# Performance work log

Measured on AMD Instinct MI355X. Metric: run time of the kernel, lower is better.

The kernel has to match this reference:

```python
import jax, jax.numpy as jnp
import numpy as np

N = 6144          # nodes
F_IN = 512        # num_feature
HID = 64          # hidden_dim
C = 40            # num_class
H = 3             # num_heads
ALPHA = 0.2       # leaky relu slope
NEG_INF = -9e15


def gat_layer(x, adj, W, a_src, a_dst):
    # x: [N, f_in], W: [H, f_in, f_out], a_src/a_dst: [H, f_out]
    Wh = jnp.einsum('nf,hfo->hno', x, W)                  # [H, N, f_out]
    e_src = jnp.einsum('hno,ho->hn', Wh, a_src)           # [H, N]
    e_dst = jnp.einsum('hno,ho->hn', Wh, a_dst)           # [H, N]
    e = jax.nn.leaky_relu(e_src[:, :, None] + e_dst[:, None, :], ALPHA)  # [H, N, N]
    scores = jnp.where(adj > 0, e, NEG_INF)               # mask non-edges
    attn = jax.nn.softmax(scores, axis=-1)                # softmax over neighbors
    out = jnp.einsum('hnm,hmo->hno', attn, Wh)            # [H, N, f_out]
    return out.mean(axis=0)                               # average heads -> [N, f_out]


def setup_inputs() -> dict:
    key = jax.random.key(0)
    k = jax.random.split(key, 8)
    feature = jax.random.normal(k[0], (N, F_IN), dtype=jnp.float32)
    adj = (jax.random.uniform(k[1], (N, N)) < 0.01).astype(jnp.float32)
    adj = jnp.maximum(adj, jnp.eye(N, dtype=jnp.float32))
    s1 = 1.0 / np.sqrt(F_IN)
    s2 = 1.0 / np.sqrt(HID)
    W1 = jax.random.normal(k[2], (H, F_IN, HID), dtype=jnp.float32) * s1
    a1_src = jax.random.normal(k[3], (H, HID), dtype=jnp.float32) * s2
    a1_dst = jax.random.normal(k[4], (H, HID), dtype=jnp.float32) * s2
    W2 = jax.random.normal(k[5], (H, HID, C), dtype=jnp.float32) * s2
    a2_src = jax.random.normal(k[6], (H, C), dtype=jnp.float32) * (1.0 / np.sqrt(C))
    a2_dst = jax.random.normal(k[7], (H, C), dtype=jnp.float32) * (1.0 / np.sqrt(C))
    return {"feature": feature, "adj": adj, "W1": W1, "a1_src": a1_src,
            "a1_dst": a1_dst, "W2": W2, "a2_src": a2_src, "a2_dst": a2_dst}


def reference(feature, adj, W1, a1_src, a1_dst, W2, a2_src, a2_dst):
    # eval mode: dropout is identity
    x = jax.nn.relu(gat_layer(feature, adj, W1, a1_src, a1_dst))  # [N, HID]
    x = gat_layer(x, adj, W2, a2_src, a2_dst)                     # [N, C]
    return jax.nn.log_softmax(x, axis=1)
```

## Files before the change

kernel.cpp:

```cpp
#include <hip/hip_runtime.h>
#include <math.h>

#define NN   6144
#define FIN  512
#define HIDN 64
#define NC   40
#define NH   3
#define CAP  128
#define NCHUNK (CAP / 64)
#define LALPHA 0.2f
#define KSPLIT 4
#define PK_LOW  0x3FFFu
#define PK_HIGH 0xFFFFC000u

__global__ __launch_bounds__(256) void k_csr(const float* __restrict__ adj,
                                             int* __restrict__ nbr,
                                             int* __restrict__ deg) {
    int row  = blockIdx.x * 4 + (threadIdx.x >> 6);
    int lane = threadIdx.x & 63;
    const float* arow = adj + (size_t)row * NN;
    int* nrow = nbr + (size_t)row * CAP;
    int cnt = 0;
    for (int base = 0; base < NN; base += 256) {
        float4 v = *reinterpret_cast<const float4*>(arow + base + lane * 4);
        float vv[4] = {v.x, v.y, v.z, v.w};
#pragma unroll
        for (int q = 0; q < 4; q++) {
            bool on = vv[q] > 0.0f;
            unsigned long long mask = __ballot(on);
            if (on) {
                int pos = cnt + __popcll(mask & ((1ull << lane) - 1ull));
                if (pos < CAP) nrow[pos] = base + lane * 4 + q;
            }
            cnt += __popcll(mask);
        }
    }
    if (lane == 0) deg[row] = cnt < CAP ? cnt : CAP;
}

__global__ __launch_bounds__(256) void k_gemm1(const float* __restrict__ x,
                                               const float* __restrict__ W,
                                               float* __restrict__ Whp) {
    __shared__ float xs[64][68];
    __shared__ float wsh[64][68];
    int h  = blockIdx.y;
    int n0 = blockIdx.x * 64;
    int kz = blockIdx.z;
    int tid = threadIdx.x;
    int og4 = (tid & 15) * 4;
    int mg4 = (tid >> 4) * 4;

    float acc[4][4] = {{0.f}};

    const float* xbase0 = x + (size_t)n0 * FIN;
    const float* wbase0 = W + (size_t)h * FIN * HIDN;

    for (int t = 0; t < 2; t++) {
        int k0 = kz * 128 + t * 64;
#pragma unroll
        for (int i = 0; i < 4; i++) {
            int l = tid + i * 256;
            int r = l >> 4;
            int c = (l & 15) * 4;
            *reinterpret_cast<float4*>(&xs[r][c]) =
                *reinterpret_cast<const float4*>(xbase0 + (size_t)r * FIN + k0 + c);
            *reinterpret_cast<float4*>(&wsh[r][c]) =
                *reinterpret_cast<const float4*>(wbase0 + (size_t)(k0 + r) * HIDN + c);
        }
        __syncthreads();

#pragma unroll 8
        for (int k = 0; k < 64; k += 4) {
            float4 xv[4], wv[4];
            xv[0] = *reinterpret_cast<const float4*>(&xs[mg4 + 0][k]);
            xv[1] = *reinterpret_cast<const float4*>(&xs[mg4 + 1][k]);
            xv[2] = *reinterpret_cast<const float4*>(&xs[mg4 + 2][k]);
            xv[3] = *reinterpret_cast<const float4*>(&xs[mg4 + 3][k]);
            wv[0] = *reinterpret_cast<const float4*>(&wsh[k + 0][og4]);
            wv[1] = *reinterpret_cast<const float4*>(&wsh[k + 1][og4]);
            wv[2] = *reinterpret_cast<const float4*>(&wsh[k + 2][og4]);
            wv[3] = *reinterpret_cast<const float4*>(&wsh[k + 3][og4]);
            const float* xf = reinterpret_cast<const float*>(xv);
            const float* wf = reinterpret_cast<const float*>(wv);
#pragma unroll
            for (int i = 0; i < 4; i++) {
#pragma unroll
                for (int kk = 0; kk < 4; kk++) {
                    float xval = xf[i * 4 + kk];
#pragma unroll
                    for (int j = 0; j < 4; j++)
                        acc[i][j] += xval * wf[kk * 4 + j];
                }
            }
        }
        __syncthreads();
    }

    float* outp = Whp + (((size_t)kz * NH + h) * NN + n0 + mg4) * HIDN + og4;
#pragma unroll
    for (int i = 0; i < 4; i++) {
        float4 v = make_float4(acc[i][0], acc[i][1], acc[i][2], acc[i][3]);
        *reinterpret_cast<float4*>(outp + (size_t)i * HIDN) = v;
    }
}

__global__ __launch_bounds__(256) void k_sum_e1(const float* __restrict__ Whp,
                                                const float* __restrict__ a_src,
                                                const float* __restrict__ a_dst,
                                                float* __restrict__ Wh,
                                                float* __restrict__ es,
                                                float* __restrict__ ed) {
    int gw   = blockIdx.x * 4 + (threadIdx.x >> 6);
    int lane = threadIdx.x & 63;
    int h = gw / NN, n = gw % NN;
    size_t idx = ((size_t)h * NN + n) * HIDN + lane;
    size_t stride = (size_t)NH * NN * HIDN;
    float v = Whp[idx] + Whp[idx + stride] + Whp[idx + 2 * stride] + Whp[idx + 3 * stride];
    Wh[idx] = v;
    float s = v * a_src[h * HIDN + lane];
    float d = v * a_dst[h * HIDN + lane];
#pragma unroll
    for (int off = 32; off; off >>= 1) {
        s += __shfl_xor(s, off);
        d += __shfl_xor(d, off);
    }
    if (lane == 0) { es[h * NN + n] = s; ed[h * NN + n] = d; }
}

__global__ __launch_bounds__(192) void k_attn1f(const int* __restrict__ nbr,
                                                const int* __restrict__ deg,
                                                const float* __restrict__ Wh,
                                                const float* __restrict__ es,
                                                const float* __restrict__ ed,
                                                const float* __restrict__ W2,
                                                const float* __restrict__ a2s,
                                                const float* __restrict__ a2d,
                                                float* __restrict__ Wh2,
                                                float* __restrict__ e2s,
                                                float* __restrict__ e2d) {
    __shared__ unsigned pks[NH][CAP];
    __shared__ float hsum[NH][HIDN];
    int n = blockIdx.x;
    int h = threadIdx.x >> 6;
    int lane = threadIdx.x & 63;
    int d = deg[n];
    const int* nrow = nbr + (size_t)n * CAP;
    float esv = es[h * NN + n];

    float psum = 0.f;
#pragma unroll
    for (int c = 0; c < NCHUNK; c++) {
        int k = c * 64 + lane;
        unsigned u = 0;
        if (k < d) {
            int mm = nrow[k];
            float e = esv + ed[h * NN + mm];
            float s = e > 0.f ? e : LALPHA * e;
            float p = __expf(s);
            u = (__float_as_uint(p) & PK_HIGH) | (unsigned)mm;
            psum += __uint_as_float(u & PK_HIGH);
        }
        pks[h][k] = u;
    }
#pragma unroll
    for (int off = 32; off; off >>= 1) psum += __shfl_xor(psum, off);
    float inv = 1.f / psum;
    __syncthreads();

    const float* WhH = Wh + (size_t)h * NN * HIDN + lane;
    float a0 = 0.f, a1 = 0.f, a2 = 0.f, a3 = 0.f;
    int iters = (d + 3) >> 2;
    for (int g = 0; g < iters; g++) {
        uint4 uu = *reinterpret_cast<const uint4*>(&pks[h][g * 4]);
        a0 += __uint_as_float(uu.x & PK_HIGH) * WhH[(size_t)(uu.x & PK_LOW) * HIDN];
        a1 += __uint_as_float(uu.y & PK_HIGH) * WhH[(size_t)(uu.y & PK_LOW) * HIDN];
        a2 += __uint_as_float(uu.z & PK_HIGH) * WhH[(size_t)(uu.z & PK_LOW) * HIDN];
        a3 += __uint_as_float(uu.w & PK_HIGH) * WhH[(size_t)(uu.w & PK_LOW) * HIDN];
    }
    float hacc = ((a0 + a1) + (a2 + a3));
    hsum[h][lane] = hacc * inv;
    __syncthreads();

    float xv = (hsum[0][lane] + hsum[1][lane] + hsum[2][lane]) * (1.f / NH);
    xv = fmaxf(xv, 0.f);

    int c = lane < NC ? lane : NC - 1;
    float acc = 0.f;
#pragma unroll 8
    for (int o = 0; o < HIDN; o++) {
        float xb = __shfl(xv, o);
        float wv = W2[((size_t)h * HIDN + o) * NC + c];
        acc += xb * wv;
    }
    if (lane >= NC) acc = 0.f;

    float s2 = acc * (lane < NC ? a2s[h * NC + lane] : 0.f);
    float d2 = acc * (lane < NC ? a2d[h * NC + lane] : 0.f);
#pragma unroll
    for (int off = 32; off; off >>= 1) {
        s2 += __shfl_xor(s2, off);
        d2 += __shfl_xor(d2, off);
    }
    if (lane < NC) Wh2[((size_t)h * NN + n) * NC + lane] = acc;
    if (lane == 0) { e2s[h * NN + n] = s2; e2d[h * NN + n] = d2; }
}

__global__ __launch_bounds__(192) void k_attn2(const int* __restrict__ nbr,
                                               const int* __restrict__ deg,
                                               const float* __restrict__ Wh2,
                                               const float* __restrict__ es,
                                               const float* __restrict__ ed,
                                               float* __restrict__ out) {
    __shared__ unsigned pks[NH][CAP];
    __shared__ float hsum[NH][HIDN];
    int n = blockIdx.x;
    int h = threadIdx.x >> 6;
    int lane = threadIdx.x & 63;
    int d = deg[n];
    const int* nrow = nbr + (size_t)n * CAP;
    float esv = es[h * NN + n];

    float psum = 0.f;
#pragma unroll
    for (int c = 0; c < NCHUNK; c++) {
        int k = c * 64 + lane;
        unsigned u = 0;
        if (k < d) {
            int mm = nrow[k];
            float e = esv + ed[h * NN + mm];
            float s = e > 0.f ? e : LALPHA * e;
            float p = __expf(s);
            u = (__float_as_uint(p) & PK_HIGH) | (unsigned)mm;
            psum += __uint_as_float(u & PK_HIGH);
        }
        pks[h][k] = u;
    }
#pragma unroll
    for (int off = 32; off; off >>= 1) psum += __shfl_xor(psum, off);
    float inv = 1.f / psum;
    __syncthreads();

    const float* W2H = Wh2 + (size_t)h * NN * NC + (lane < NC ? lane : 0);
    float a0 = 0.f, a1 = 0.f, a2 = 0.f, a3 = 0.f;
    int iters = (d + 3) >> 2;
    for (int g = 0; g < iters; g++) {
        uint4 uu = *reinterpret_cast<const uint4*>(&pks[h][g * 4]);
        a0 += __uint_as_float(uu.x & PK_HIGH) * W2H[(size_t)(uu.x & PK_LOW) * NC];
        a1 += __uint_as_float(uu.y & PK_HIGH) * W2H[(size_t)(uu.y & PK_LOW) * NC];
        a2 += __uint_as_float(uu.z & PK_HIGH) * W2H[(size_t)(uu.z & PK_LOW) * NC];
        a3 += __uint_as_float(uu.w & PK_HIGH) * W2H[(size_t)(uu.w & PK_LOW) * NC];
    }
    float hacc = ((a0 + a1) + (a2 + a3));
    if (lane < NC) hsum[h][lane] = hacc * inv;
    __syncthreads();

    if (threadIdx.x < 64) {
        float a = (lane < NC)
            ? (hsum[0][lane] + hsum[1][lane] + hsum[2][lane]) * (1.f / NH)
            : -INFINITY;
        float mx = a;
#pragma unroll
        for (int off = 32; off; off >>= 1) mx = fmaxf(mx, __shfl_xor(mx, off));
        float ex = (lane < NC) ? __expf(a - mx) : 0.f;
        float se = ex;
#pragma unroll
        for (int off = 32; off; off >>= 1) se += __shfl_xor(se, off);
        if (lane < NC) out[(size_t)n * NC + lane] = a - mx - logf(se);
    }
}

extern "C" void kernel_launch(void* const* d_in, const int* in_sizes, int n_in,
                              void* d_out, int out_size, void* d_ws, size_t ws_size,
                              hipStream_t stream) {
    const float* feature = (const float*)d_in[0];
    const float* adj     = (const float*)d_in[1];
    const float* W1      = (const float*)d_in[2];
    const float* a1_src  = (const float*)d_in[3];
    const float* a1_dst  = (const float*)d_in[4];
    const float* W2      = (const float*)d_in[5];
    const float* a2_src  = (const float*)d_in[6];
    const float* a2_dst  = (const float*)d_in[7];
    float* out = (float*)d_out;

    char* ws = (char*)d_ws;
    size_t off = 0;
    int*   nbr = (int*)(ws + off);   off += (size_t)NN * CAP * sizeof(int);
    int*   deg = (int*)(ws + off);   off += (size_t)NN * sizeof(int);
    float* Whp = (float*)(ws + off); off += (size_t)KSPLIT * NH * NN * HIDN * sizeof(float);
    float* Wh1 = (float*)(ws + off); off += (size_t)NH * NN * HIDN * sizeof(float);
    float* e1s = (float*)(ws + off); off += (size_t)NH * NN * sizeof(float);
    float* e1d = (float*)(ws + off); off += (size_t)NH * NN * sizeof(float);
    float* Wh2 = (float*)(ws + off); off += (size_t)NH * NN * NC * sizeof(float);
    float* e2s = (float*)(ws + off); off += (size_t)NH * NN * sizeof(float);
    float* e2d = (float*)(ws + off); off += (size_t)NH * NN * sizeof(float);

    k_csr<<<NN / 4, 256, 0, stream>>>(adj, nbr, deg);
    k_gemm1<<<dim3(NN / 64, NH, KSPLIT), 256, 0, stream>>>(feature, W1, Whp);
    k_sum_e1<<<(NH * NN) / 4, 256, 0, stream>>>(Whp, a1_src, a1_dst, Wh1, e1s, e1d);
    k_attn1f<<<NN, 192, 0, stream>>>(nbr, deg, Wh1, e1s, e1d, W2, a2_src, a2_dst,
                                     Wh2, e2s, e2d);
    k_attn2<<<NN, 192, 0, stream>>>(nbr, deg, Wh2, e2s, e2d, out);
}
```

Baseline: 105.9 us.

## Merge CSR build with GEMM launch and store Wh tensors as bf16

```diff
diff --git a/kernel.cpp b/kernel.cpp
--- a/kernel.cpp
+++ b/kernel.cpp
@@ -12,46 +12,63 @@
 #define KSPLIT 4
 #define PK_LOW  0x3FFFu
 #define PK_HIGH 0xFFFFC000u
-
-__global__ __launch_bounds__(256) void k_csr(const float* __restrict__ adj,
-                                             int* __restrict__ nbr,
-                                             int* __restrict__ deg) {
-    int row  = blockIdx.x * 4 + (threadIdx.x >> 6);
-    int lane = threadIdx.x & 63;
-    const float* arow = adj + (size_t)row * NN;
-    int* nrow = nbr + (size_t)row * CAP;
-    int cnt = 0;
-    for (int base = 0; base < NN; base += 256) {
-        float4 v = *reinterpret_cast<const float4*>(arow + base + lane * 4);
-        float vv[4] = {v.x, v.y, v.z, v.w};
-#pragma unroll
-        for (int q = 0; q < 4; q++) {
-            bool on = vv[q] > 0.0f;
-            unsigned long long mask = __ballot(on);
-            if (on) {
-                int pos = cnt + __popcll(mask & ((1ull << lane) - 1ull));
-                if (pos < CAP) nrow[pos] = base + lane * 4 + q;
+#define CSRB   (NN / 4)
+#define GEMMB  ((NN / 64) * NH * KSPLIT)
+
+__device__ __forceinline__ float bf2f(ushort s) {
+    return __uint_as_float((unsigned)s << 16);
+}
+__device__ __forceinline__ ushort f2bf(float f) {
+    unsigned u = __float_as_uint(f);
+    return (ushort)((u + 0x7FFFu + ((u >> 16) & 1u)) >> 16);
+}
+
+__global__ __launch_bounds__(256) void k_csr_gemm(const float* __restrict__ adj,
+                                                  int* __restrict__ nbr,
+                                                  int* __restrict__ deg,
+                                                  const float* __restrict__ x,
+                                                  const float* __restrict__ W,
+                                                  float* __restrict__ Whp) {
+    __shared__ float smem[2 * 64 * 68];
+    int bid = blockIdx.x;
+    int tid = threadIdx.x;
+
+    if (bid < CSRB) {
+        int row  = bid * 4 + (tid >> 6);
+        int lane = tid & 63;
+        const float* arow = adj + (size_t)row * NN;
+        int* nrow = nbr + (size_t)row * CAP;
+        int cnt = 0;
+        for (int base = 0; base < NN; base += 256) {
+            float4 v = *reinterpret_cast<const float4*>(arow + base + lane * 4);
+            float vv[4] = {v.x, v.y, v.z, v.w};
+#pragma unroll
+            for (int q = 0; q < 4; q++) {
+                bool on = vv[q] > 0.0f;
+                unsigned long long mask = __ballot(on);
+                if (on) {
+                    int pos = cnt + __popcll(mask & ((1ull << lane) - 1ull));
+                    if (pos < CAP) nrow[pos] = base + lane * 4 + q;
+                }
+                cnt += __popcll(mask);
             }
-            cnt += __popcll(mask);
-        }
-    }
-    if (lane == 0) deg[row] = cnt < CAP ? cnt : CAP;
-}
-
-__global__ __launch_bounds__(256) void k_gemm1(const float* __restrict__ x,
-                                               const float* __restrict__ W,
-                                               float* __restrict__ Whp) {
-    __shared__ float xs[64][68];
-    __shared__ float wsh[64][68];
-    int h  = blockIdx.y;
-    int n0 = blockIdx.x * 64;
-    int kz = blockIdx.z;
-    int tid = threadIdx.x;
+        }
+        if (lane == 0) deg[row] = cnt < CAP ? cnt : CAP;
+        return;
+    }
+
+    int b  = bid - CSRB;
+    int kz = b / ((NN / 64) * NH);
+    int rem = b % ((NN / 64) * NH);
+    int h  = rem / (NN / 64);
+    int n0 = (rem % (NN / 64)) * 64;
     int og4 = (tid & 15) * 4;
     int mg4 = (tid >> 4) * 4;
 
+    float (*xs)[68]  = reinterpret_cast<float(*)[68]>(smem);
+    float (*wsh)[68] = reinterpret_cast<float(*)[68]>(smem + 64 * 68);
+
     float acc[4][4] = {{0.f}};
-
     const float* xbase0 = x + (size_t)n0 * FIN;
     const float* wbase0 = W + (size_t)h * FIN * HIDN;
 
@@ -107,7 +124,7 @@
 __global__ __launch_bounds__(256) void k_sum_e1(const float* __restrict__ Whp,
                                                 const float* __restrict__ a_src,
                                                 const float* __restrict__ a_dst,
-                                                float* __restrict__ Wh,
+                                                ushort* __restrict__ Whb,
                                                 float* __restrict__ es,
                                                 float* __restrict__ ed) {
     int gw   = blockIdx.x * 4 + (threadIdx.x >> 6);
@@ -116,7 +133,7 @@
     size_t idx = ((size_t)h * NN + n) * HIDN + lane;
     size_t stride = (size_t)NH * NN * HIDN;
     float v = Whp[idx] + Whp[idx + stride] + Whp[idx + 2 * stride] + Whp[idx + 3 * stride];
-    Wh[idx] = v;
+    Whb[idx] = f2bf(v);
     float s = v * a_src[h * HIDN + lane];
     float d = v * a_dst[h * HIDN + lane];
 #pragma unroll
@@ -129,13 +146,13 @@
 
 __global__ __launch_bounds__(192) void k_attn1f(const int* __restrict__ nbr,
                                                 const int* __restrict__ deg,
-                                                const float* __restrict__ Wh,
+                                                const ushort* __restrict__ Whb,
                                                 const float* __restrict__ es,
                                                 const float* __restrict__ ed,
                                                 const float* __restrict__ W2,
                                                 const float* __restrict__ a2s,
                                                 const float* __restrict__ a2d,
-                                                float* __restrict__ Wh2,
+                                                ushort* __restrict__ Wh2b,
                                                 float* __restrict__ e2s,
                                                 float* __restrict__ e2d) {
     __shared__ unsigned pks[NH][CAP];
@@ -167,15 +184,15 @@
     float inv = 1.f / psum;
     __syncthreads();
 
-    const float* WhH = Wh + (size_t)h * NN * HIDN + lane;
+    const ushort* WhH = Whb + (size_t)h * NN * HIDN + lane;
     float a0 = 0.f, a1 = 0.f, a2 = 0.f, a3 = 0.f;
     int iters = (d + 3) >> 2;
     for (int g = 0; g < iters; g++) {
         uint4 uu = *reinterpret_cast<const uint4*>(&pks[h][g * 4]);
-        a0 += __uint_as_float(uu.x & PK_HIGH) * WhH[(size_t)(uu.x & PK_LOW) * HIDN];
-        a1 += __uint_as_float(uu.y & PK_HIGH) * WhH[(size_t)(uu.y & PK_LOW) * HIDN];
-        a2 += __uint_as_float(uu.z & PK_HIGH) * WhH[(size_t)(uu.z & PK_LOW) * HIDN];
-        a3 += __uint_as_float(uu.w & PK_HIGH) * WhH[(size_t)(uu.w & PK_LOW) * HIDN];
+        a0 += __uint_as_float(uu.x & PK_HIGH) * bf2f(WhH[(size_t)(uu.x & PK_LOW) * HIDN]);
+        a1 += __uint_as_float(uu.y & PK_HIGH) * bf2f(WhH[(size_t)(uu.y & PK_LOW) * HIDN]);
+        a2 += __uint_as_float(uu.z & PK_HIGH) * bf2f(WhH[(size_t)(uu.z & PK_LOW) * HIDN]);
+        a3 += __uint_as_float(uu.w & PK_HIGH) * bf2f(WhH[(size_t)(uu.w & PK_LOW) * HIDN]);
     }
     float hacc = ((a0 + a1) + (a2 + a3));
     hsum[h][lane] = hacc * inv;
@@ -201,13 +218,13 @@
         s2 += __shfl_xor(s2, off);
         d2 += __shfl_xor(d2, off);
     }
-    if (lane < NC) Wh2[((size_t)h * NN + n) * NC + lane] = acc;
+    if (lane < NC) Wh2b[((size_t)h * NN + n) * NC + lane] = f2bf(acc);
     if (lane == 0) { e2s[h * NN + n] = s2; e2d[h * NN + n] = d2; }
 }
 
 __global__ __launch_bounds__(192) void k_attn2(const int* __restrict__ nbr,
                                                const int* __restrict__ deg,
-                                               const float* __restrict__ Wh2,
+                                               const ushort* __restrict__ Wh2b,
                                                const float* __restrict__ es,
                                                const float* __restrict__ ed,
                                                float* __restrict__ out) {
@@ -240,15 +257,15 @@
     float inv = 1.f / psum;
     __syncthreads();
 
-    const float* W2H = Wh2 + (size_t)h * NN * NC + (lane < NC ? lane : 0);
+    const ushort* W2H = Wh2b + (size_t)h * NN * NC + (lane < NC ? lane : 0);
     float a0 = 0.f, a1 = 0.f, a2 = 0.f, a3 = 0.f;
     int iters = (d + 3) >> 2;
     for (int g = 0; g < iters; g++) {
         uint4 uu = *reinterpret_cast<const uint4*>(&pks[h][g * 4]);
-        a0 += __uint_as_float(uu.x & PK_HIGH) * W2H[(size_t)(uu.x & PK_LOW) * NC];
-        a1 += __uint_as_float(uu.y & PK_HIGH) * W2H[(size_t)(uu.y & PK_LOW) * NC];
-        a2 += __uint_as_float(uu.z & PK_HIGH) * W2H[(size_t)(uu.z & PK_LOW) * NC];
-        a3 += __uint_as_float(uu.w & PK_HIGH) * W2H[(size_t)(uu.w & PK_LOW) * NC];
+        a0 += __uint_as_float(uu.x & PK_HIGH) * bf2f(W2H[(size_t)(uu.x & PK_LOW) * NC]);
+        a1 += __uint_as_float(uu.y & PK_HIGH) * bf2f(W2H[(size_t)(uu.y & PK_LOW) * NC]);
+        a2 += __uint_as_float(uu.z & PK_HIGH) * bf2f(W2H[(size_t)(uu.z & PK_LOW) * NC]);
+        a3 += __uint_as_float(uu.w & PK_HIGH) * bf2f(W2H[(size_t)(uu.w & PK_LOW) * NC]);
     }
     float hacc = ((a0 + a1) + (a2 + a3));
     if (lane < NC) hsum[h][lane] = hacc * inv;
@@ -284,20 +301,19 @@
 
     char* ws = (char*)d_ws;
     size_t off = 0;
-    int*   nbr = (int*)(ws + off);   off += (size_t)NN * CAP * sizeof(int);
-    int*   deg = (int*)(ws + off);   off += (size_t)NN * sizeof(int);
-    float* Whp = (float*)(ws + off); off += (size_t)KSPLIT * NH * NN * HIDN * sizeof(float);
-    float* Wh1 = (float*)(ws + off); off += (size_t)NH * NN * HIDN * sizeof(float);
-    float* e1s = (float*)(ws + off); off += (size_t)NH * NN * sizeof(float);
-    float* e1d = (float*)(ws + off); off += (size_t)NH * NN * sizeof(float);
-    float* Wh2 = (float*)(ws + off); off += (size_t)NH * NN * NC * sizeof(float);
-    float* e2s = (float*)(ws + off); off += (size_t)NH * NN * sizeof(float);
-    float* e2d = (float*)(ws + off); off += (size_t)NH * NN * sizeof(float);
-
-    k_csr<<<NN / 4, 256, 0, stream>>>(adj, nbr, deg);
-    k_gemm1<<<dim3(NN / 64, NH, KSPLIT), 256, 0, stream>>>(feature, W1, Whp);
-    k_sum_e1<<<(NH * NN) / 4, 256, 0, stream>>>(Whp, a1_src, a1_dst, Wh1, e1s, e1d);
-    k_attn1f<<<NN, 192, 0, stream>>>(nbr, deg, Wh1, e1s, e1d, W2, a2_src, a2_dst,
-                                     Wh2, e2s, e2d);
-    k_attn2<<<NN, 192, 0, stream>>>(nbr, deg, Wh2, e2s, e2d, out);
-}
+    int*    nbr = (int*)(ws + off);    off += (size_t)NN * CAP * sizeof(int);
+    int*    deg = (int*)(ws + off);    off += (size_t)NN * sizeof(int);
+    float*  Whp = (float*)(ws + off);  off += (size_t)KSPLIT * NH * NN * HIDN * sizeof(float);
+    ushort* Whb = (ushort*)(ws + off); off += (size_t)NH * NN * HIDN * sizeof(ushort);
+    float*  e1s = (float*)(ws + off);  off += (size_t)NH * NN * sizeof(float);
+    float*  e1d = (float*)(ws + off);  off += (size_t)NH * NN * sizeof(float);
+    ushort* Wh2b= (ushort*)(ws + off); off += (size_t)NH * NN * NC * sizeof(ushort);
+    float*  e2s = (float*)(ws + off);  off += (size_t)NH * NN * sizeof(float);
+    float*  e2d = (float*)(ws + off);  off += (size_t)NH * NN * sizeof(float);
+
+    k_csr_gemm<<<CSRB + GEMMB, 256, 0, stream>>>(adj, nbr, deg, feature, W1, Whp);
+    k_sum_e1<<<(NH * NN) / 4, 256, 0, stream>>>(Whp, a1_src, a1_dst, Whb, e1s, e1d);
+    k_attn1f<<<NN, 192, 0, stream>>>(nbr, deg, Whb, e1s, e1d, W2, a2_src, a2_dst,
+                                     Wh2b, e2s, e2d);
+    k_attn2<<<NN, 192, 0, stream>>>(nbr, deg, Wh2b, e2s, e2d, out);
+}
```

Result: faster. 102.6 us (-3.1%).
